# Optimization experiments

Hardware: AMD Instinct MI355X
Metric: run time of the kernel (lower is better)

## Reference

```python
import jax, jax.numpy as jnp
import numpy as np

B, T, E = 32, 2048, 128

def setup_inputs() -> dict:
    key = jax.random.key(0)
    ks = jax.random.split(key, 6)
    return {
        "x1": jax.random.normal(ks[0], (B, T, E), dtype=jnp.float32),
        "x2": jax.random.normal(ks[1], (B, T, E), dtype=jnp.float32),
        "W1": jax.random.normal(ks[2], (E, 1), dtype=jnp.float32) * 0.05,
        "b1": jnp.zeros((T, 1), dtype=jnp.float32),
        "U1": jax.random.normal(ks[3], (E, T), dtype=jnp.float32) * 0.05,
        "W2": jax.random.normal(ks[4], (E, 1), dtype=jnp.float32) * 0.05,
        "b2": jnp.zeros((T, 1), dtype=jnp.float32),
        "U2": jax.random.normal(ks[5], (E, T), dtype=jnp.float32) * 0.05,
    }


def reference(x1, x2, W1, b1, U1, W2, b2, U2):
    # S[b,i,j] = <x1[b,i], x2[b,j]>  -> (B, T, T)
    S = jnp.einsum('bie,bje->bij', x1, x2)
    inv_T = jnp.float32(1.0) / S.shape[1]
    # c1 = mean_j sum_i S[b,i,j] * x2[b,i,e]  -> (B, E)
    c1 = jnp.einsum('bij,bie->be', S, x2) * inv_T
    # c2 = mean_i sum_j S[b,i,j] * x1[b,j,e]  -> (B, E)
    c2 = jnp.einsum('bij,bje->be', S, x1) * inv_T
    # attention logits: (B, T)
    et1 = c1 @ U1 + jnp.squeeze(x1 @ W1 + b1, axis=-1)
    et2 = c2 @ U2 + jnp.squeeze(x2 @ W2 + b2, axis=-1)
    at1 = jax.nn.softmax(et1, axis=-1)
    at2 = jax.nn.softmax(et2, axis=-1)
    # attention-weighted sums: (B, E)
    o1 = jnp.einsum('bt,bte->be', at1, x1)
    o2 = jnp.einsum('bt,bte->be', at2, x2)
    # merge_mode == 'concat'
    return jnp.concatenate([o1, o2], axis=1)
```

## Files before the change

### kernel.cpp

```cpp
#include <hip/hip_runtime.h>


#define B_ 32
#define T_ 2048
#define E_ 128
#define INV_T (1.0f/2048.0f)

#define WS_SX1 0
#define WS_SX2 (B_*E_)
#define WS_C1  (2*B_*E_)
#define WS_C2  (3*B_*E_)
#define WS_ET1 (4*B_*E_)
#define WS_ET2 (4*B_*E_ + B_*T_)
#define WS_SM  (4*B_*E_ + 2*B_*T_)

__global__ void k1_colsum(const float* __restrict__ x1, const float* __restrict__ x2,
                          float* __restrict__ ws) {
    int b = blockIdx.x, chunk = blockIdx.y;
    int tid = threadIdx.x;
    int e   = tid & (E_ - 1);
    int sel = tid >> 7;
    const float* x = sel ? x2 : x1;
    float* sx = ws + (sel ? WS_SX2 : WS_SX1);
    int t0 = chunk * 128;
    const float* p = x + ((size_t)b * T_ + t0) * E_ + e;
    float acc = 0.f;
    #pragma unroll 8
    for (int r = 0; r < 128; ++r) acc += p[(size_t)r * E_];
    atomicAdd(&sx[b * E_ + e], acc);
}

__global__ void k2_wc(const float* __restrict__ x1, const float* __restrict__ x2,
                      const float* __restrict__ W1, const float* __restrict__ b1,
                      const float* __restrict__ W2, const float* __restrict__ b2,
                      float* __restrict__ ws) {
    __shared__ float s_sx1[E_], s_sx2[E_], s_W1[E_], s_W2[E_];
    __shared__ float s_w1[256], s_w2[256];
    int b = blockIdx.x, chunk = blockIdx.y;
    int tid = threadIdx.x;
    float* c1  = ws + WS_C1;
    float* c2  = ws + WS_C2;
    float* et1 = ws + WS_ET1;
    float* et2 = ws + WS_ET2;
    if (tid < E_) {
        s_sx1[tid] = ws[WS_SX1 + b * E_ + tid];
        s_sx2[tid] = ws[WS_SX2 + b * E_ + tid];
        s_W1[tid]  = W1[tid];
        s_W2[tid]  = W2[tid];
    }
    __syncthreads();

    int t0  = chunk * 256;
    int row = t0 + tid;
    const float4* r1   = (const float4*)(x1 + ((size_t)b * T_ + row) * E_);
    const float4* r2   = (const float4*)(x2 + ((size_t)b * T_ + row) * E_);
    const float4* ssx1 = (const float4*)s_sx1;
    const float4* ssx2 = (const float4*)s_sx2;
    const float4* sW1v = (const float4*)s_W1;
    const float4* sW2v = (const float4*)s_W2;
    float w1 = 0.f, xw1 = 0.f, w2 = 0.f, xw2 = 0.f;
    #pragma unroll 8
    for (int i = 0; i < E_ / 4; ++i) {
        float4 a = r1[i], s = ssx2[i], wv = sW1v[i];
        w1  += a.x * s.x  + a.y * s.y  + a.z * s.z  + a.w * s.w;
        xw1 += a.x * wv.x + a.y * wv.y + a.z * wv.z + a.w * wv.w;
        float4 c = r2[i], u = ssx1[i], vv = sW2v[i];
        w2  += c.x * u.x  + c.y * u.y  + c.z * u.z  + c.w * u.w;
        xw2 += c.x * vv.x + c.y * vv.y + c.z * vv.z + c.w * vv.w;
    }
    s_w1[tid] = w1;
    s_w2[tid] = w2;
    et1[(size_t)b * T_ + row] = xw1 + b1[row];
    et2[(size_t)b * T_ + row] = xw2 + b2[row];
    __syncthreads();

    int e   = tid & (E_ - 1);
    int sel = tid >> 7;
    float acc = 0.f;
    if (sel == 0) {
        const float* p = x2 + ((size_t)b * T_ + t0) * E_ + e;
        #pragma unroll 8
        for (int r = 0; r < 256; ++r) acc += s_w1[r] * p[(size_t)r * E_];
        atomicAdd(&c1[b * E_ + e], acc * INV_T);
    } else {
        const float* p = x1 + ((size_t)b * T_ + t0) * E_ + e;
        #pragma unroll 8
        for (int r = 0; r < 256; ++r) acc += s_w2[r] * p[(size_t)r * E_];
        atomicAdd(&c2[b * E_ + e], acc * INV_T);
    }
}

__global__ void k3_et(const float* __restrict__ U1, const float* __restrict__ U2,
                      float* __restrict__ ws) {
    __shared__ float s_c1[E_], s_c2[E_];
    int b = blockIdx.x, chunk = blockIdx.y;
    int tid = threadIdx.x;
    float* et1 = ws + WS_ET1;
    float* et2 = ws + WS_ET2;
    if (tid < E_) s_c1[tid] = ws[WS_C1 + b * E_ + tid];
    else          s_c2[tid - E_] = ws[WS_C2 + b * E_ + tid - E_];
    __syncthreads();
    int t = chunk * 256 + tid;
    float a1 = et1[(size_t)b * T_ + t];
    float a2 = et2[(size_t)b * T_ + t];
    #pragma unroll 8
    for (int e = 0; e < E_; ++e) {
        a1 += s_c1[e] * U1[(size_t)e * T_ + t];
        a2 += s_c2[e] * U2[(size_t)e * T_ + t];
    }
    et1[(size_t)b * T_ + t] = a1;
    et2[(size_t)b * T_ + t] = a2;
}

__global__ void k4_softmax_reduce(float* __restrict__ ws) {
    __shared__ float red[256];
    int b   = blockIdx.x >> 1;
    int sel = blockIdx.x & 1;
    int tid = threadIdx.x;
    const float* et = ws + (sel ? WS_ET2 : WS_ET1) + (size_t)b * T_;
    float v[8];
    float m = -3.4e38f;
    #pragma unroll
    for (int k = 0; k < 8; ++k) { v[k] = et[tid + k * 256]; m = fmaxf(m, v[k]); }
    red[tid] = m; __syncthreads();
    for (int s = 128; s > 0; s >>= 1) {
        if (tid < s) red[tid] = fmaxf(red[tid], red[tid + s]);
        __syncthreads();
    }
    m = red[0]; __syncthreads();
    float l = 0.f;
    #pragma unroll
    for (int k = 0; k < 8; ++k) l += __expf(v[k] - m);
    red[tid] = l; __syncthreads();
    for (int s = 128; s > 0; s >>= 1) {
        if (tid < s) red[tid] += red[tid + s];
        __syncthreads();
    }
    if (tid == 0) {
        float* sm = ws + WS_SM + sel * 2 * B_;
        sm[b]       = m;
        sm[B_ + b]  = red[0];
    }
}

__global__ void k5_out(const float* __restrict__ x1, const float* __restrict__ x2,
                       const float* __restrict__ ws, float* __restrict__ out) {
    __shared__ float s_p1[256], s_p2[256];
    int b = blockIdx.x, chunk = blockIdx.y;
    int tid = threadIdx.x;
    const float* et1 = ws + WS_ET1;
    const float* et2 = ws + WS_ET2;
    const float* sm  = ws + WS_SM;
    float m1 = sm[b],          il1 = 1.f / sm[B_ + b];
    float m2 = sm[2 * B_ + b], il2 = 1.f / sm[3 * B_ + b];
    int t0 = chunk * 256;
    s_p1[tid] = __expf(et1[(size_t)b * T_ + t0 + tid] - m1) * il1;
    s_p2[tid] = __expf(et2[(size_t)b * T_ + t0 + tid] - m2) * il2;
    __syncthreads();
    int e   = tid & (E_ - 1);
    int sel = tid >> 7;
    float acc = 0.f;
    if (sel == 0) {
        const float* p = x1 + ((size_t)b * T_ + t0) * E_ + e;
        #pragma unroll 8
        for (int r = 0; r < 256; ++r) acc += s_p1[r] * p[(size_t)r * E_];
        atomicAdd(&out[b * 2 * E_ + e], acc);
    } else {
        const float* p = x2 + ((size_t)b * T_ + t0) * E_ + e;
        #pragma unroll 8
        for (int r = 0; r < 256; ++r) acc += s_p2[r] * p[(size_t)r * E_];
        atomicAdd(&out[b * 2 * E_ + E_ + e], acc);
    }
}

extern "C" void kernel_launch(void* const* d_in, const int* in_sizes, int n_in,
                              void* d_out, int out_size, void* d_ws, size_t ws_size,
                              hipStream_t stream) {
    const float* x1 = (const float*)d_in[0];
    const float* x2 = (const float*)d_in[1];
    const float* W1 = (const float*)d_in[2];
    const float* b1 = (const float*)d_in[3];
    const float* U1 = (const float*)d_in[4];
    const float* W2 = (const float*)d_in[5];
    const float* b2 = (const float*)d_in[6];
    const float* U2 = (const float*)d_in[7];
    float* ws  = (float*)d_ws;
    float* out = (float*)d_out;

    hipMemsetAsync(ws, 0, (size_t)4 * B_ * E_ * sizeof(float), stream);
    hipMemsetAsync(out, 0, (size_t)2 * B_ * E_ * sizeof(float), stream);

    k1_colsum<<<dim3(B_, 16), 256, 0, stream>>>(x1, x2, ws);
    k2_wc<<<dim3(B_, 8), 256, 0, stream>>>(x1, x2, W1, b1, W2, b2, ws);
    k3_et<<<dim3(B_, 8), 256, 0, stream>>>(U1, U2, ws);
    k4_softmax_reduce<<<2 * B_, 256, 0, stream>>>(ws);
    k5_out<<<dim3(B_, 8), 256, 0, stream>>>(x1, x2, ws, out);
}
```

Measured before the change: 162.4 us.

## Rewrite pipeline with float4 coalesced loads, register reuse, and fused softmax

Every kernel is rewritten. Row reductions now use float4 loads with wave-wide and shared-memory tree reductions instead of one column per thread, and the grid grows from 8 to 32 chunks per batch for more parallelism. k2 keeps its x rows in registers and reuses them for the second weighted sum instead of reading x again. The logit and softmax kernels are fused so normalized probabilities are written directly, and two memsets are replaced by a single zeroing kernel. This reduces strided uncoalesced traffic and launch count, but adds more atomics and lowers occupancy in the fused softmax kernel (64 blocks).

```diff
diff --git a/kernel.cpp b/kernel.cpp
--- a/kernel.cpp
+++ b/kernel.cpp
@@ -4,6 +4,7 @@
 #define B_ 32
 #define T_ 2048
 #define E_ 128
+#define EV (E_/4)
 #define INV_T (1.0f/2048.0f)
 
 #define WS_SX1 0
@@ -12,164 +13,227 @@
 #define WS_C2  (3*B_*E_)
 #define WS_ET1 (4*B_*E_)
 #define WS_ET2 (4*B_*E_ + B_*T_)
-#define WS_SM  (4*B_*E_ + 2*B_*T_)
-
-__global__ void k1_colsum(const float* __restrict__ x1, const float* __restrict__ x2,
-                          float* __restrict__ ws) {
-    int b = blockIdx.x, chunk = blockIdx.y;
-    int tid = threadIdx.x;
-    int e   = tid & (E_ - 1);
-    int sel = tid >> 7;
-    const float* x = sel ? x2 : x1;
-    float* sx = ws + (sel ? WS_SX2 : WS_SX1);
-    int t0 = chunk * 128;
-    const float* p = x + ((size_t)b * T_ + t0) * E_ + e;
-    float acc = 0.f;
-    #pragma unroll 8
-    for (int r = 0; r < 128; ++r) acc += p[(size_t)r * E_];
-    atomicAdd(&sx[b * E_ + e], acc);
-}
-
-__global__ void k2_wc(const float* __restrict__ x1, const float* __restrict__ x2,
-                      const float* __restrict__ W1, const float* __restrict__ b1,
-                      const float* __restrict__ W2, const float* __restrict__ b2,
-                      float* __restrict__ ws) {
-    __shared__ float s_sx1[E_], s_sx2[E_], s_W1[E_], s_W2[E_];
-    __shared__ float s_w1[256], s_w2[256];
-    int b = blockIdx.x, chunk = blockIdx.y;
-    int tid = threadIdx.x;
-    float* c1  = ws + WS_C1;
-    float* c2  = ws + WS_C2;
-    float* et1 = ws + WS_ET1;
-    float* et2 = ws + WS_ET2;
+#define WS_ACC_N (4*B_*E_)
+#define OUT_N (2*B_*E_)
+
+__device__ __forceinline__ float dot4(float4 a, float4 b) {
+    return a.x*b.x + a.y*b.y + a.z*b.z + a.w*b.w;
+}
+__device__ __forceinline__ void fma4(float4& a, float s, const float4 v) {
+    a.x += s*v.x; a.y += s*v.y; a.z += s*v.z; a.w += s*v.w;
+}
+__device__ __forceinline__ void add4(float4& a, const float4 v) {
+    a.x += v.x; a.y += v.y; a.z += v.z; a.w += v.w;
+}
+
+__global__ void k0_zero(float* __restrict__ ws, float* __restrict__ out) {
+    int i = blockIdx.x * 256 + threadIdx.x;
+    if (i < WS_ACC_N) ws[i] = 0.f;
+    else               out[i - WS_ACC_N] = 0.f;
+}
+
+__global__ __launch_bounds__(256)
+void k1_sx(const float* __restrict__ x1, const float* __restrict__ x2,
+           float* __restrict__ ws) {
+    __shared__ float4 s_r1[256], s_r2[256];
+    const int b = blockIdx.x, ch = blockIdx.y, tid = threadIdx.x;
+    const float4* p1 = (const float4*)x1 + ((size_t)b*T_ + ch*64)*EV;
+    const float4* p2 = (const float4*)x2 + ((size_t)b*T_ + ch*64)*EV;
+    const int rg = tid >> 5, q = tid & 31;
+    float4 a1 = {0,0,0,0}, a2 = {0,0,0,0};
+    #pragma unroll
+    for (int i = 0; i < 8; ++i) {
+        int r = i*8 + rg;
+        add4(a1, p1[r*EV + q]);
+        add4(a2, p2[r*EV + q]);
+    }
+    s_r1[tid] = a1; s_r2[tid] = a2;
+    __syncthreads();
+    for (int s = 128; s >= 32; s >>= 1) {
+        if (tid < s) { add4(s_r1[tid], s_r1[tid+s]); add4(s_r2[tid], s_r2[tid+s]); }
+        __syncthreads();
+    }
+    if (tid < 32) {
+        float4 t1 = s_r1[tid], t2 = s_r2[tid];
+        atomicAdd(&ws[WS_SX1 + b*E_ + tid*4+0], t1.x);
+        atomicAdd(&ws[WS_SX1 + b*E_ + tid*4+1], t1.y);
+        atomicAdd(&ws[WS_SX1 + b*E_ + tid*4+2], t1.z);
+        atomicAdd(&ws[WS_SX1 + b*E_ + tid*4+3], t1.w);
+        atomicAdd(&ws[WS_SX2 + b*E_ + tid*4+0], t2.x);
+        atomicAdd(&ws[WS_SX2 + b*E_ + tid*4+1], t2.y);
+        atomicAdd(&ws[WS_SX2 + b*E_ + tid*4+2], t2.z);
+        atomicAdd(&ws[WS_SX2 + b*E_ + tid*4+3], t2.w);
+    }
+}
+
+__global__ __launch_bounds__(256)
+void k2_wc(const float* __restrict__ x1, const float* __restrict__ x2,
+           const float* __restrict__ W1, const float* __restrict__ b1,
+           const float* __restrict__ W2, const float* __restrict__ b2,
+           float* __restrict__ ws) {
+    __shared__ float4 s_r1[256], s_r2[256];
+    __shared__ float  s_a[E_], s_b[E_], s_wa[E_], s_wb[E_];
+    __shared__ float  s_w1[64], s_w2[64];
+    const int b = blockIdx.x, ch = blockIdx.y, tid = threadIdx.x;
     if (tid < E_) {
-        s_sx1[tid] = ws[WS_SX1 + b * E_ + tid];
-        s_sx2[tid] = ws[WS_SX2 + b * E_ + tid];
-        s_W1[tid]  = W1[tid];
-        s_W2[tid]  = W2[tid];
-    }
-    __syncthreads();
-
-    int t0  = chunk * 256;
-    int row = t0 + tid;
-    const float4* r1   = (const float4*)(x1 + ((size_t)b * T_ + row) * E_);
-    const float4* r2   = (const float4*)(x2 + ((size_t)b * T_ + row) * E_);
-    const float4* ssx1 = (const float4*)s_sx1;
-    const float4* ssx2 = (const float4*)s_sx2;
-    const float4* sW1v = (const float4*)s_W1;
-    const float4* sW2v = (const float4*)s_W2;
-    float w1 = 0.f, xw1 = 0.f, w2 = 0.f, xw2 = 0.f;
-    #pragma unroll 8
-    for (int i = 0; i < E_ / 4; ++i) {
-        float4 a = r1[i], s = ssx2[i], wv = sW1v[i];
-        w1  += a.x * s.x  + a.y * s.y  + a.z * s.z  + a.w * s.w;
-        xw1 += a.x * wv.x + a.y * wv.y + a.z * wv.z + a.w * wv.w;
-        float4 c = r2[i], u = ssx1[i], vv = sW2v[i];
-        w2  += c.x * u.x  + c.y * u.y  + c.z * u.z  + c.w * u.w;
-        xw2 += c.x * vv.x + c.y * vv.y + c.z * vv.z + c.w * vv.w;
-    }
-    s_w1[tid] = w1;
-    s_w2[tid] = w2;
-    et1[(size_t)b * T_ + row] = xw1 + b1[row];
-    et2[(size_t)b * T_ + row] = xw2 + b2[row];
-    __syncthreads();
-
-    int e   = tid & (E_ - 1);
-    int sel = tid >> 7;
-    float acc = 0.f;
-    if (sel == 0) {
-        const float* p = x2 + ((size_t)b * T_ + t0) * E_ + e;
-        #pragma unroll 8
-        for (int r = 0; r < 256; ++r) acc += s_w1[r] * p[(size_t)r * E_];
-        atomicAdd(&c1[b * E_ + e], acc * INV_T);
-    } else {
-        const float* p = x1 + ((size_t)b * T_ + t0) * E_ + e;
-        #pragma unroll 8
-        for (int r = 0; r < 256; ++r) acc += s_w2[r] * p[(size_t)r * E_];
-        atomicAdd(&c2[b * E_ + e], acc * INV_T);
-    }
-}
-
-__global__ void k3_et(const float* __restrict__ U1, const float* __restrict__ U2,
-                      float* __restrict__ ws) {
-    __shared__ float s_c1[E_], s_c2[E_];
-    int b = blockIdx.x, chunk = blockIdx.y;
-    int tid = threadIdx.x;
-    float* et1 = ws + WS_ET1;
-    float* et2 = ws + WS_ET2;
-    if (tid < E_) s_c1[tid] = ws[WS_C1 + b * E_ + tid];
-    else          s_c2[tid - E_] = ws[WS_C2 + b * E_ + tid - E_];
-    __syncthreads();
-    int t = chunk * 256 + tid;
-    float a1 = et1[(size_t)b * T_ + t];
-    float a2 = et2[(size_t)b * T_ + t];
-    #pragma unroll 8
+        s_a[tid]  = ws[WS_SX1 + b*E_ + tid];
+        s_b[tid]  = ws[WS_SX2 + b*E_ + tid];
+        s_wa[tid] = W1[tid];
+        s_wb[tid] = W2[tid];
+    }
+    __syncthreads();
+    const float4* p1 = (const float4*)x1 + ((size_t)b*T_ + ch*64)*EV;
+    const float4* p2 = (const float4*)x2 + ((size_t)b*T_ + ch*64)*EV;
+    const float4* sx1v = (const float4*)s_a;
+    const float4* sx2v = (const float4*)s_b;
+    const float4* W1v  = (const float4*)s_wa;
+    const float4* W2v  = (const float4*)s_wb;
+    const int wv = tid >> 6, l = tid & 63;
+    const int rp = l >> 5, q = l & 31;
+    const int rowoff = wv*2 + rp;
+
+    float4 v1[8], v2[8];
+    #pragma unroll
+    for (int i = 0; i < 8; ++i) {
+        int r = i*8 + rowoff;
+        v1[i] = p1[r*EV + q];
+        v2[i] = p2[r*EV + q];
+    }
+
+    float* et1 = ws + WS_ET1 + (size_t)b*T_ + ch*64;
+    float* et2 = ws + WS_ET2 + (size_t)b*T_ + ch*64;
+    #pragma unroll
+    for (int i = 0; i < 8; ++i) {
+        int r = i*8 + rowoff;
+        float pw1 = dot4(v1[i], sx2v[q]);
+        float px1 = dot4(v1[i], W1v[q]);
+        float pw2 = dot4(v2[i], sx1v[q]);
+        float px2 = dot4(v2[i], W2v[q]);
+        #pragma unroll
+        for (int m = 1; m <= 16; m <<= 1) {
+            pw1 += __shfl_xor(pw1, m);
+            px1 += __shfl_xor(px1, m);
+            pw2 += __shfl_xor(pw2, m);
+            px2 += __shfl_xor(px2, m);
+        }
+        if (q == 0) {
+            s_w1[r] = pw1; s_w2[r] = pw2;
+            int trow = ch*64 + r;
+            et1[r] = px1 + b1[trow];
+            et2[r] = px2 + b2[trow];
+        }
+    }
+    __syncthreads();
+
+    float4 a1 = {0,0,0,0}, a2 = {0,0,0,0};
+    #pragma unroll
+    for (int i = 0; i < 8; ++i) {
+        int r = i*8 + rowoff;
+        fma4(a1, s_w1[r], v2[i]);
+        fma4(a2, s_w2[r], v1[i]);
+    }
+    s_r1[tid] = a1; s_r2[tid] = a2;
+    __syncthreads();
+    for (int s = 128; s >= 32; s >>= 1) {
+        if (tid < s) { add4(s_r1[tid], s_r1[tid+s]); add4(s_r2[tid], s_r2[tid+s]); }
+        __syncthreads();
+    }
+    if (tid < 32) {
+        float4 t1 = s_r1[tid], t2 = s_r2[tid];
+        atomicAdd(&ws[WS_C1 + b*E_ + tid*4+0], t1.x * INV_T);
+        atomicAdd(&ws[WS_C1 + b*E_ + tid*4+1], t1.y * INV_T);
+        atomicAdd(&ws[WS_C1 + b*E_ + tid*4+2], t1.z * INV_T);
+        atomicAdd(&ws[WS_C1 + b*E_ + tid*4+3], t1.w * INV_T);
+        atomicAdd(&ws[WS_C2 + b*E_ + tid*4+0], t2.x * INV_T);
+        atomicAdd(&ws[WS_C2 + b*E_ + tid*4+1], t2.y * INV_T);
+        atomicAdd(&ws[WS_C2 + b*E_ + tid*4+2], t2.z * INV_T);
+        atomicAdd(&ws[WS_C2 + b*E_ + tid*4+3], t2.w * INV_T);
+    }
+}
+
+__global__ __launch_bounds__(256)
+void k3_et_softmax(const float* __restrict__ U1, const float* __restrict__ U2,
+                   float* __restrict__ ws) {
+    __shared__ float s_c[E_];
+    __shared__ float red[256];
+    const int b = blockIdx.x, sel = blockIdx.y, tid = threadIdx.x;
+    const float* U = sel ? U2 : U1;
+    const float* cp = ws + (sel ? WS_C2 : WS_C1) + b*E_;
+    float4* et4 = (float4*)(ws + (sel ? WS_ET2 : WS_ET1) + (size_t)b*T_);
+    if (tid < E_) s_c[tid] = cp[tid];
+    __syncthreads();
+    const float4* U4 = (const float4*)U;
+    float4 acc0 = et4[tid];
+    float4 acc1 = et4[tid + 256];
+    #pragma unroll 4
     for (int e = 0; e < E_; ++e) {
-        a1 += s_c1[e] * U1[(size_t)e * T_ + t];
-        a2 += s_c2[e] * U2[(size_t)e * T_ + t];
-    }
-    et1[(size_t)b * T_ + t] = a1;
-    et2[(size_t)b * T_ + t] = a2;
-}
-
-__global__ void k4_softmax_reduce(float* __restrict__ ws) {
-    __shared__ float red[256];
-    int b   = blockIdx.x >> 1;
-    int sel = blockIdx.x & 1;
-    int tid = threadIdx.x;
-    const float* et = ws + (sel ? WS_ET2 : WS_ET1) + (size_t)b * T_;
-    float v[8];
-    float m = -3.4e38f;
-    #pragma unroll
-    for (int k = 0; k < 8; ++k) { v[k] = et[tid + k * 256]; m = fmaxf(m, v[k]); }
+        float ce = s_c[e];
+        fma4(acc0, ce, U4[(size_t)e*(T_/4) + tid]);
+        fma4(acc1, ce, U4[(size_t)e*(T_/4) + tid + 256]);
+    }
+    float m = fmaxf(fmaxf(fmaxf(acc0.x, acc0.y), fmaxf(acc0.z, acc0.w)),
+                    fmaxf(fmaxf(acc1.x, acc1.y), fmaxf(acc1.z, acc1.w)));
     red[tid] = m; __syncthreads();
     for (int s = 128; s > 0; s >>= 1) {
-        if (tid < s) red[tid] = fmaxf(red[tid], red[tid + s]);
+        if (tid < s) red[tid] = fmaxf(red[tid], red[tid+s]);
         __syncthreads();
     }
     m = red[0]; __syncthreads();
-    float l = 0.f;
-    #pragma unroll
-    for (int k = 0; k < 8; ++k) l += __expf(v[k] - m);
-    red[tid] = l; __syncthreads();
+    float4 e0, e1;
+    e0.x = __expf(acc0.x - m); e0.y = __expf(acc0.y - m);
+    e0.z = __expf(acc0.z - m); e0.w = __expf(acc0.w - m);
+    e1.x = __expf(acc1.x - m); e1.y = __expf(acc1.y - m);
+    e1.z = __expf(acc1.z - m); e1.w = __expf(acc1.w - m);
+    float lsum = e0.x + e0.y + e0.z + e0.w + e1.x + e1.y + e1.z + e1.w;
+    red[tid] = lsum; __syncthreads();
     for (int s = 128; s > 0; s >>= 1) {
-        if (tid < s) red[tid] += red[tid + s];
-        __syncthreads();
-    }
-    if (tid == 0) {
-        float* sm = ws + WS_SM + sel * 2 * B_;
-        sm[b]       = m;
-        sm[B_ + b]  = red[0];
-    }
-}
-
-__global__ void k5_out(const float* __restrict__ x1, const float* __restrict__ x2,
-                       const float* __restrict__ ws, float* __restrict__ out) {
-    __shared__ float s_p1[256], s_p2[256];
-    int b = blockIdx.x, chunk = blockIdx.y;
-    int tid = threadIdx.x;
-    const float* et1 = ws + WS_ET1;
-    const float* et2 = ws + WS_ET2;
-    const float* sm  = ws + WS_SM;
-    float m1 = sm[b],          il1 = 1.f / sm[B_ + b];
-    float m2 = sm[2 * B_ + b], il2 = 1.f / sm[3 * B_ + b];
-    int t0 = chunk * 256;
-    s_p1[tid] = __expf(et1[(size_t)b * T_ + t0 + tid] - m1) * il1;
-    s_p2[tid] = __expf(et2[(size_t)b * T_ + t0 + tid] - m2) * il2;
-    __syncthreads();
-    int e   = tid & (E_ - 1);
-    int sel = tid >> 7;
-    float acc = 0.f;
-    if (sel == 0) {
-        const float* p = x1 + ((size_t)b * T_ + t0) * E_ + e;
-        #pragma unroll 8
-        for (int r = 0; r < 256; ++r) acc += s_p1[r] * p[(size_t)r * E_];
-        atomicAdd(&out[b * 2 * E_ + e], acc);
-    } else {
-        const float* p = x2 + ((size_t)b * T_ + t0) * E_ + e;
-        #pragma unroll 8
-        for (int r = 0; r < 256; ++r) acc += s_p2[r] * p[(size_t)r * E_];
-        atomicAdd(&out[b * 2 * E_ + E_ + e], acc);
+        if (tid < s) red[tid] += red[tid+s];
+        __syncthreads();
+    }
+    float il = 1.f / red[0];
+    e0.x *= il; e0.y *= il; e0.z *= il; e0.w *= il;
+    e1.x *= il; e1.y *= il; e1.z *= il; e1.w *= il;
+    et4[tid]       = e0;
+    et4[tid + 256] = e1;
+}
+
+__global__ __launch_bounds__(256)
+void k5_out(const float* __restrict__ x1, const float* __restrict__ x2,
+            const float* __restrict__ ws, float* __restrict__ out) {
+    __shared__ float4 s_r1[256], s_r2[256];
+    __shared__ float s_p1[64], s_p2[64];
+    const int b = blockIdx.x, ch = blockIdx.y, tid = threadIdx.x;
+    const float* pr1 = ws + WS_ET1 + (size_t)b*T_ + ch*64;
+    const float* pr2 = ws + WS_ET2 + (size_t)b*T_ + ch*64;
+    if (tid < 64)        s_p1[tid] = pr1[tid];
+    else if (tid < 128)  s_p2[tid - 64] = pr2[tid - 64];
+    __syncthreads();
+    const float4* p1 = (const float4*)x1 + ((size_t)b*T_ + ch*64)*EV;
+    const float4* p2 = (const float4*)x2 + ((size_t)b*T_ + ch*64)*EV;
+    const int rg = tid >> 5, q = tid & 31;
+    float4 a1 = {0,0,0,0}, a2 = {0,0,0,0};
+    #pragma unroll
+    for (int i = 0; i < 8; ++i) {
+        int r = i*8 + rg;
+        fma4(a1, s_p1[r], p1[r*EV + q]);
+        fma4(a2, s_p2[r], p2[r*EV + q]);
+    }
+    s_r1[tid] = a1; s_r2[tid] = a2;
+    __syncthreads();
+    for (int s = 128; s >= 32; s >>= 1) {
+        if (tid < s) { add4(s_r1[tid], s_r1[tid+s]); add4(s_r2[tid], s_r2[tid+s]); }
+        __syncthreads();
+    }
+    if (tid < 32) {
+        float4 t1 = s_r1[tid], t2 = s_r2[tid];
+        atomicAdd(&out[b*2*E_ + tid*4+0], t1.x);
+        atomicAdd(&out[b*2*E_ + tid*4+1], t1.y);
+        atomicAdd(&out[b*2*E_ + tid*4+2], t1.z);
+        atomicAdd(&out[b*2*E_ + tid*4+3], t1.w);
+        atomicAdd(&out[b*2*E_ + E_ + tid*4+0], t2.x);
+        atomicAdd(&out[b*2*E_ + E_ + tid*4+1], t2.y);
+        atomicAdd(&out[b*2*E_ + E_ + tid*4+2], t2.z);
+        atomicAdd(&out[b*2*E_ + E_ + tid*4+3], t2.w);
     }
 }
 
@@ -187,12 +251,9 @@
     float* ws  = (float*)d_ws;
     float* out = (float*)d_out;
 
-    hipMemsetAsync(ws, 0, (size_t)4 * B_ * E_ * sizeof(float), stream);
-    hipMemsetAsync(out, 0, (size_t)2 * B_ * E_ * sizeof(float), stream);
-
-    k1_colsum<<<dim3(B_, 16), 256, 0, stream>>>(x1, x2, ws);
-    k2_wc<<<dim3(B_, 8), 256, 0, stream>>>(x1, x2, W1, b1, W2, b2, ws);
-    k3_et<<<dim3(B_, 8), 256, 0, stream>>>(U1, U2, ws);
-    k4_softmax_reduce<<<2 * B_, 256, 0, stream>>>(ws);
-    k5_out<<<dim3(B_, 8), 256, 0, stream>>>(x1, x2, ws, out);
-}
+    k0_zero<<<dim3((WS_ACC_N + OUT_N) / 256), 256, 0, stream>>>(ws, out);
+    k1_sx<<<dim3(B_, 32), 256, 0, stream>>>(x1, x2, ws);
+    k2_wc<<<dim3(B_, 32), 256, 0, stream>>>(x1, x2, W1, b1, W2, b2, ws);
+    k3_et_softmax<<<dim3(B_, 2), 256, 0, stream>>>(U1, U2, ws);
+    k5_out<<<dim3(B_, 32), 256, 0, stream>>>(x1, x2, ws, out);
+}
```

Measured after the change: 155.1 us. 1.05x faster.
